# Optimization experiments

Hardware: AMD Instinct MI355X
Metric: run time of the kernel (lower is better)

## Reference

```python
import jax, jax.numpy as jnp
import numpy as np

B, P, C, H, W = 256, 512, 512, 7, 8
T = H * W  # 56
EPS = 1e-8


def setup_inputs() -> dict:
    key = jax.random.key(0)
    k1, k2, k3 = jax.random.split(key, 3)
    inp = jax.random.normal(k1, (B, C, H, W), dtype=jnp.float32)
    # xavier-uniform-like init for prototype (fan over last two dims as torch does)
    bound_p = float(np.sqrt(6.0 / (P + C * T)))
    prototype = jax.random.uniform(k2, (P, C, T), dtype=jnp.float32, minval=-bound_p, maxval=bound_p)
    bound_w = float(np.sqrt(6.0 / (C + 1)))
    fc_w = jax.random.uniform(k3, (1, C), dtype=jnp.float32, minval=-bound_w, maxval=bound_w)
    fc_b = jnp.zeros((1,), dtype=jnp.float32)
    return {"input": inp, "prototype": prototype, "fc_w": fc_w, "fc_b": fc_b}


def reference(input, prototype, fc_w, fc_b):
    # flatten spatial dims: (B, C, T)
    x = input.reshape(input.shape[0], input.shape[1], -1)
    # per-position cosine similarity over channel dim
    dots = jnp.einsum('bct,pct->bpt', x, prototype)          # (B, P, T)
    xn = jnp.linalg.norm(x, axis=1)                           # (B, T)
    pn = jnp.linalg.norm(prototype, axis=1)                   # (P, T)
    sim = dots / jnp.maximum(xn[:, None, :] * pn[None, :, :], EPS)
    att = jax.nn.softmax(sim, axis=-1)                        # (B, P, T)
    # attention-pooled elementwise product: (B, P, C)
    feat = jnp.einsum('bpt,bct,pct->bpc', att, x, prototype)
    # fc: Linear(C, 1) then relu, view to (B, P)
    out = jax.nn.relu(jnp.einsum('bpc,oc->bpo', feat, fc_w) + fc_b)
    return out.reshape(out.shape[0], out.shape[1])
```

## Files before the change

kernel.cpp:

```cpp
#include <hip/hip_runtime.h>
#include <hip/hip_bf16.h>
#include <math.h>

constexpr int kB = 256, kC = 512, kT = 56, kP = 512;
constexpr int kCT = kC * kT;

typedef short v4s __attribute__((ext_vector_type(4)));
typedef short v8s __attribute__((ext_vector_type(8)));
typedef float v4f __attribute__((ext_vector_type(4)));
typedef float v16f __attribute__((ext_vector_type(16)));

__device__ __forceinline__ unsigned pack_bf16(float a, float b) {
  __hip_bfloat16 ha = __float2bfloat16(a);
  __hip_bfloat16 hb = __float2bfloat16(b);
  unsigned short ua, ub;
  __builtin_memcpy(&ua, &ha, 2);
  __builtin_memcpy(&ub, &hb, 2);
  return (unsigned)ua | ((unsigned)ub << 16);
}

__device__ __forceinline__ v4s frag2(unsigned w0, unsigned w1) {
  unsigned u[2] = {w0, w1};
  v4s s;
  __builtin_memcpy(&s, u, 8);
  return s;
}

__device__ __forceinline__ v8s frag8(uint4 u) {
  v8s s;
  __builtin_memcpy(&s, &u, 16);
  return s;
}

#define GLOAD(gp, lp)                                                        \
  __builtin_amdgcn_global_load_lds(                                          \
      (const __attribute__((address_space(1))) unsigned*)(const unsigned*)(gp), \
      (__attribute__((address_space(3))) unsigned*)(unsigned*)(lp), 16, 0, 0)

__global__ __launch_bounds__(512) void prep_kernel(
    const float* __restrict__ x, const float* __restrict__ proto,
    const float* __restrict__ fcw,
    unsigned* __restrict__ xt, unsigned* __restrict__ xwt,
    unsigned* __restrict__ pt,
    float* __restrict__ xn, float* __restrict__ pn) {
  __shared__ float tile[128 * 57];
  __shared__ float fws[512];
  __shared__ float part[8][64];

  const int tid = threadIdx.x;
  const int n = blockIdx.x;
  const bool isx = (n < kB);
  const int row = isx ? n : (n - kB);
  const float* src = (isx ? x : proto) + (size_t)row * kCT;

  fws[tid] = fcw[tid & 511];

  const int g = tid >> 6, tt = tid & 63;
  float nacc = 0.f;

#pragma unroll 1
  for (int ch = 0; ch < 4; ++ch) {
    const float* csrc = src + ch * (128 * 56);
#pragma unroll
    for (int it = 0; it < 4; ++it) {
      const int idx = it * 512 + tid;
      if (idx < 1792) {
        const int f0 = idx * 4;
        float4 v = *(const float4*)(csrc + f0);
        int c = (int)(((unsigned)f0 * 74899u) >> 22);
        int t = f0 - c * 56;
        tile[c * 57 + t] = v.x;
        tile[c * 57 + t + 1] = v.y;
        tile[c * 57 + t + 2] = v.z;
        tile[c * 57 + t + 3] = v.w;
      }
    }
    __syncthreads();
    if (tt < 56) {
#pragma unroll
      for (int cc2 = 0; cc2 < 16; ++cc2) {
        float u = tile[(g * 16 + cc2) * 57 + tt];
        nacc = fmaf(u, u, nacc);
      }
    }
#pragma unroll
    for (int it = 0; it < 7; ++it) {
      const int id = it * 512 + tid;
      const int t = id >> 6;
      const int cw = id & 63;
      float g0 = tile[(2 * cw) * 57 + t];
      float g1 = tile[(2 * cw + 1) * 57 + t];
      unsigned wd = pack_bf16(g0, g1);
      if (isx) {
        const size_t o = ((size_t)(t * kB + row)) * 256 + ch * 64 + cw;
        const int c = ch * 128 + 2 * cw;
        xt[o] = wd;
        xwt[o] = pack_bf16(g0 * fws[c], g1 * fws[c + 1]);
      } else {
        pt[((size_t)(t * kP + row)) * 256 + ch * 64 + cw] = wd;
      }
    }
    __syncthreads();
  }

  part[g][tt] = nacc;
  __syncthreads();
  if (tid < 56) {
    float s = 0.f;
#pragma unroll
    for (int gg = 0; gg < 8; ++gg) s += part[gg][tid];
    float r = sqrtf(s);
    if (isx) xn[row * 56 + tid] = r; else pn[row * 56 + tid] = r;
  }
}

constexpr int TILE = 64 * 64;
constexpr int BUFW = 3 * TILE;

__global__ __launch_bounds__(256) void proto_gemm_kernel(
    const unsigned* __restrict__ xt, const unsigned* __restrict__ xwt,
    const unsigned* __restrict__ pt,
    const float* __restrict__ xn, const float* __restrict__ pn,
    float* __restrict__ part) {
  __shared__ __align__(16) unsigned lds[2 * BUFW];
  __shared__ float xnL[7 * 64], pnL[7 * 64];

  const int tid = threadIdx.x;
  const int l = tid & 63;
  const int w4 = tid >> 6;
  const int wm = w4 >> 1;
  const int wn = w4 & 1;

  int bid = (int)blockIdx.x;
  bid = (bid & 7) * 32 + (bid >> 3);
  const int b0 = (bid & 3) * 64;
  const int p0 = ((bid >> 2) & 7) * 64;
  const int tg = bid >> 5;

  for (int i = tid; i < 7 * 64; i += 256) {
    const int tl = i >> 6, r = i & 63;
    xnL[i] = xn[(b0 + r) * 56 + tg * 7 + tl];
    pnL[i] = pn[(p0 + r) * 56 + tg * 7 + tl];
  }

  const int l16 = l >> 4, s16 = l & 15;
  size_t xro[4], pro[4];
  int lo[4];
#pragma unroll
  for (int jj = 0; jj < 4; ++jj) {
    const int row = w4 * 16 + jj * 4 + l16;
    const int ch4 = (s16 ^ (row & 7)) * 4;
    xro[jj] = (size_t)(b0 + row) * 256 + ch4;
    pro[jj] = (size_t)(p0 + row) * 256 + ch4;
    lo[jj] = (w4 * 16 + jj * 4) * 64;
  }

  const int fr = l & 31;
  const int hi = l >> 5;
  const int sw4 = (l & 7) * 4;
  const int axb = (wm * 32 + fr) * 64;
  const int pxb = (wn * 32 + fr) * 64;

  v16f aD, aW, sac, nac;
#pragma unroll
  for (int i = 0; i < 16; ++i) { aD[i] = 0.f; aW[i] = 0.f; sac[i] = 0.f; nac[i] = 0.f; }

  auto STAGE = [&](int s, int buf) {
    const int t = tg * 7 + (s >> 2);
    const size_t xoff = (size_t)t * (kB * 256) + (size_t)((s & 3) * 64);
    const size_t poff = (size_t)t * (kP * 256) + (size_t)((s & 3) * 64);
    unsigned* lb = lds + buf * BUFW;
#pragma unroll
    for (int jj = 0; jj < 4; ++jj) {
      GLOAD(xt + xro[jj] + xoff, lb + lo[jj]);
      GLOAD(xwt + xro[jj] + xoff, lb + TILE + lo[jj]);
      GLOAD(pt + pro[jj] + poff, lb + 2 * TILE + lo[jj]);
    }
  };

  auto COMPUTE = [&](int s) {
    const unsigned* bx = lds + (s & 1) * BUFW;
#pragma unroll
    for (int ks = 0; ks < 8; ++ks) {
      const int col = (ks * 8 + hi * 4) ^ sw4;
      v8s xf = frag8(*(const uint4*)(bx + axb + col));
      v8s wf = frag8(*(const uint4*)(bx + TILE + axb + col));
      v8s pf = frag8(*(const uint4*)(bx + 2 * TILE + pxb + col));
      aD = __builtin_amdgcn_mfma_f32_32x32x16_bf16(xf, pf, aD, 0, 0, 0);
      aW = __builtin_amdgcn_mfma_f32_32x32x16_bf16(wf, pf, aW, 0, 0, 0);
    }
    if ((s & 3) == 3) {
      const int tl = s >> 2;
      const float pnv = pnL[tl * 64 + wn * 32 + fr];
#pragma unroll
      for (int i = 0; i < 16; ++i) {
        const int drow = (i & 3) + 8 * (i >> 2) + 4 * hi;
        float xnv = xnL[tl * 64 + wm * 32 + drow];
        float den = fmaxf(xnv * pnv, 1e-8f);
        float sim = aD[i] * __builtin_amdgcn_rcpf(den);
        float e = __expf(sim);
        sac[i] += e;
        nac[i] = fmaf(e, aW[i], nac[i]);
        aD[i] = 0.f;
        aW[i] = 0.f;
      }
    }
  };

  STAGE(0, 0);
  __syncthreads();

#pragma unroll 1
  for (int s = 0; s < 28; ++s) {
    if (s < 27) STAGE(s + 1, (s + 1) & 1);
    COMPUTE(s);
    __syncthreads();
  }

  float* psb = part + ((size_t)tg * 2 + 0) * 131072;
  float* pnb = part + ((size_t)tg * 2 + 1) * 131072;
#pragma unroll
  for (int i = 0; i < 16; ++i) {
    const int drow = (i & 3) + 8 * (i >> 2) + 4 * hi;
    const size_t o = (size_t)(b0 + wm * 32 + drow) * 512 + p0 + wn * 32 + fr;
    psb[o] = sac[i];
    pnb[o] = nac[i];
  }
}

__global__ __launch_bounds__(256) void merge_kernel(
    const float* __restrict__ part, const float* __restrict__ fcb,
    float* __restrict__ out) {
  const int pair = blockIdx.x * 256 + threadIdx.x;
  float S = 0.f, N = 0.f;
#pragma unroll
  for (int k = 0; k < 8; ++k) {
    S += part[((size_t)k * 2 + 0) * 131072 + pair];
    N += part[((size_t)k * 2 + 1) * 131072 + pair];
  }
  float o = N * __builtin_amdgcn_rcpf(S) + fcb[0];
  out[pair] = fmaxf(o, 0.f);
}

__global__ __launch_bounds__(1024) void proto_mfma_kernel(
    const float* __restrict__ x, const float* __restrict__ proto,
    const float* __restrict__ fcw, const float* __restrict__ fcb,
    float* __restrict__ out) {
  __shared__ unsigned xs[56 * 289];
  __shared__ unsigned ps[56 * 145];
  __shared__ unsigned pws[56 * 145];

  const int tid = threadIdx.x;
  const int l = tid & 63;
  const int w = tid >> 6;
  const int bq = w & 1;
  const int tq = w >> 1;
  const int t0 = tq * 7;

  const int n = blockIdx.y * 32 + blockIdx.x;
  const int p0 = (n >> 3) * 16;
  const int b0 = (n & 7) * 32;

  const bool act = (l < 56);
  const int lt = l;

  const int xbase0 = ((b0 + 2 * w + 0) * kC) * kT + lt;
  const int xbase1 = ((b0 + 2 * w + 1) * kC) * kT + lt;
  const int pbase = ((p0 + w) * kC) * kT + lt;

  const int arow = l & 15;
  const int q2 = (l >> 4) << 1;
  const int xoff = (bq * 16 + arow) * 9 + q2;
  const int poff = arow * 9 + q2;

  v4f acc[7][2];
#pragma unroll
  for (int ti = 0; ti < 7; ++ti) {
    acc[ti][0] = v4f{0.f, 0.f, 0.f, 0.f};
    acc[ti][1] = v4f{0.f, 0.f, 0.f, 0.f};
  }
  float xn2a = 0.f, xn2b = 0.f, pn2 = 0.f;

#pragma unroll 1
  for (int st = 0; st < 32; ++st) {
    const int k0 = st * 16;
    if (act) {
#pragma unroll
      for (int r = 0; r < 16; ++r) {
        const int cw = r & 7;
        const int c = k0 + 2 * cw;
        const int ga = ((r >> 3) ? xbase1 : xbase0) + c * kT;
        float g0 = x[ga], g1 = x[ga + kT];
        if (r >> 3) xn2b = fmaf(g0, g0, fmaf(g1, g1, xn2b));
        else xn2a = fmaf(g0, g0, fmaf(g1, g1, xn2a));
        xs[lt * 289 + (2 * w + (r >> 3)) * 9 + cw] = pack_bf16(g0, g1);
      }
#pragma unroll
      for (int cw = 0; cw < 8; ++cw) {
        const int c = k0 + 2 * cw;
        const int ga = pbase + c * kT;
        float g0 = proto[ga], g1 = proto[ga + kT];
        pn2 = fmaf(g0, g0, fmaf(g1, g1, pn2));
        ps[lt * 145 + w * 9 + cw] = pack_bf16(g0, g1);
        float f0 = fcw[c], f1 = fcw[c + 1];
        pws[lt * 145 + w * 9 + cw] = pack_bf16(g0 * f0, g1 * f1);
      }
    }
    __syncthreads();
#pragma unroll
    for (int ti = 0; ti < 7; ++ti) {
      const int t = t0 + ti;
      unsigned xw0 = xs[t * 289 + xoff];
      unsigned xw1 = xs[t * 289 + xoff + 1];
      unsigned pw0 = ps[t * 145 + poff];
      unsigned pw1 = ps[t * 145 + poff + 1];
      unsigned ww0 = pws[t * 145 + poff];
      unsigned ww1 = pws[t * 145 + poff + 1];
      v4s af = frag2(xw0, xw1);
      v4s bf = frag2(pw0, pw1);
      v4s wf = frag2(ww0, ww1);
      acc[ti][0] = __builtin_amdgcn_mfma_f32_16x16x16bf16_1k(af, bf, acc[ti][0], 0, 0, 0);
      acc[ti][1] = __builtin_amdgcn_mfma_f32_16x16x16bf16_1k(af, wf, acc[ti][1], 0, 0, 0);
    }
    __syncthreads();
  }

  float* xnorm = (float*)ps;
  float* pnorm = xnorm + 32 * 56;
  if (act) {
    xnorm[(2 * w + 0) * 56 + lt] = xn2a;
    xnorm[(2 * w + 1) * 56 + lt] = xn2b;
    pnorm[w * 56 + lt] = pn2;
  }
  __syncthreads();

  float* fm = (float*)xs;
  float* fsum = fm + 4096;
  float* fnum = fsum + 4096;
  const int pc = arow;
  const int qq = l >> 4;
#pragma unroll
  for (int i = 0; i < 4; ++i) {
    const int bl = bq * 16 + 4 * qq + i;
    float m = -3.0e38f;
    float sims[7];
#pragma unroll
    for (int ti = 0; ti < 7; ++ti) {
      const int t = t0 + ti;
      float den = fmaxf(sqrtf(xnorm[bl * 56 + t]) * sqrtf(pnorm[pc * 56 + t]), 1e-8f);
      float s = acc[ti][0][i] / den;
      sims[ti] = s;
      m = fmaxf(m, s);
    }
    float se = 0.f, nu = 0.f;
#pragma unroll
    for (int ti = 0; ti < 7; ++ti) {
      float e = __expf(sims[ti] - m);
      se += e;
      nu = fmaf(e, acc[ti][1][i], nu);
    }
    const int pair = bl * 16 + pc;
    fm[tq * 512 + pair] = m;
    fsum[tq * 512 + pair] = se;
    fnum[tq * 512 + pair] = nu;
  }
  __syncthreads();

  if (tid < 512) {
    float M = -3.0e38f;
#pragma unroll
    for (int k = 0; k < 8; ++k) M = fmaxf(M, fm[k * 512 + tid]);
    float S = 0.f, N = 0.f;
#pragma unroll
    for (int k = 0; k < 8; ++k) {
      float sc = __expf(fm[k * 512 + tid] - M);
      S = fmaf(fsum[k * 512 + tid], sc, S);
      N = fmaf(fnum[k * 512 + tid], sc, N);
    }
    float o = N / S + fcb[0];
    out[(b0 + (tid >> 4)) * kP + p0 + (tid & 15)] = fmaxf(o, 0.f);
  }
}

extern "C" void kernel_launch(void* const* d_in, const int* in_sizes, int n_in,
                              void* d_out, int out_size, void* d_ws, size_t ws_size,
                              hipStream_t stream) {
  const float* x = (const float*)d_in[0];
  const float* proto = (const float*)d_in[1];
  const float* fcw = (const float*)d_in[2];
  const float* fcb = (const float*)d_in[3];
  float* out = (float*)d_out;

  const size_t need = 67280896;
  if (ws_size >= need) {
    unsigned* xt = (unsigned*)d_ws;
    unsigned* xwt = xt + 3670016;
    unsigned* ptb = xt + 7340032;
    float* partb = (float*)(xt + 14680064);
    float* xnb = (float*)(xt + 16777216);
    float* pnb = xnb + 14336;

    hipLaunchKernelGGL(prep_kernel, dim3(kB + kP), dim3(512), 0, stream,
                       x, proto, fcw, xt, xwt, ptb, xnb, pnb);
    hipLaunchKernelGGL(proto_gemm_kernel, dim3(256), dim3(256), 0, stream,
                       xt, xwt, ptb, xnb, pnb, partb);
    hipLaunchKernelGGL(merge_kernel, dim3(512), dim3(256), 0, stream,
                       partb, fcb, out);
  } else {
    hipLaunchKernelGGL(proto_mfma_kernel, dim3(32, 8), dim3(1024), 0, stream,
                       x, proto, fcw, fcb, out);
  }
}
```

Before: 76.03 us.

## Split time groups finer, shrink K-tile, add triple-buffered async pipeline in gemm

```diff
diff --git a/kernel.cpp b/kernel.cpp
--- a/kernel.cpp
+++ b/kernel.cpp
@@ -114,16 +114,16 @@
   }
 }
 
-constexpr int TILE = 64 * 64;
-constexpr int BUFW = 3 * TILE;
-
-__global__ __launch_bounds__(256) void proto_gemm_kernel(
+constexpr int TILE = 64 * 32;
+constexpr int BUF = 3 * TILE;
+
+__global__ __launch_bounds__(256, 2) void proto_gemm_kernel(
     const unsigned* __restrict__ xt, const unsigned* __restrict__ xwt,
     const unsigned* __restrict__ pt,
     const float* __restrict__ xn, const float* __restrict__ pn,
     float* __restrict__ part) {
-  __shared__ __align__(16) unsigned lds[2 * BUFW];
-  __shared__ float xnL[7 * 64], pnL[7 * 64];
+  __shared__ __align__(16) unsigned lds[3 * BUF];
+  __shared__ float xnL[4 * 64], pnL[4 * 64];
 
   const int tid = threadIdx.x;
   const int l = tid & 63;
@@ -132,65 +132,66 @@
   const int wn = w4 & 1;
 
   int bid = (int)blockIdx.x;
-  bid = (bid & 7) * 32 + (bid >> 3);
+  bid = (bid & 7) * 56 + (bid >> 3);
   const int b0 = (bid & 3) * 64;
   const int p0 = ((bid >> 2) & 7) * 64;
   const int tg = bid >> 5;
 
-  for (int i = tid; i < 7 * 64; i += 256) {
-    const int tl = i >> 6, r = i & 63;
-    xnL[i] = xn[(b0 + r) * 56 + tg * 7 + tl];
-    pnL[i] = pn[(p0 + r) * 56 + tg * 7 + tl];
-  }
-
-  const int l16 = l >> 4, s16 = l & 15;
-  size_t xro[4], pro[4];
-  int lo[4];
-#pragma unroll
-  for (int jj = 0; jj < 4; ++jj) {
-    const int row = w4 * 16 + jj * 4 + l16;
-    const int ch4 = (s16 ^ (row & 7)) * 4;
-    xro[jj] = (size_t)(b0 + row) * 256 + ch4;
-    pro[jj] = (size_t)(p0 + row) * 256 + ch4;
-    lo[jj] = (w4 * 16 + jj * 4) * 64;
+  {
+    const int tl = tid >> 6, r = tid & 63;
+    xnL[tid] = xn[(b0 + r) * 56 + tg * 4 + tl];
+    pnL[tid] = pn[(p0 + r) * 56 + tg * 4 + tl];
+  }
+  __syncthreads();
+
+  const int lrow = l >> 3, lch = l & 7;
+  size_t xsrc[2], psrc[2];
+  int ldst[2];
+#pragma unroll
+  for (int j = 0; j < 2; ++j) {
+    const int row = w4 * 16 + j * 8 + lrow;
+    const int ch4 = ((lch ^ (row & 7))) * 4;
+    xsrc[j] = (size_t)(b0 + row) * 256 + ch4;
+    psrc[j] = (size_t)(p0 + row) * 256 + ch4;
+    ldst[j] = (w4 * 16 + j * 8) * 32;
   }
 
   const int fr = l & 31;
   const int hi = l >> 5;
-  const int sw4 = (l & 7) * 4;
-  const int axb = (wm * 32 + fr) * 64;
-  const int pxb = (wn * 32 + fr) * 64;
+  const int axb = (wm * 32 + fr) * 32;
+  const int pxb = (wn * 32 + fr) * 32;
+  const int frs = fr & 7;
 
   v16f aD, aW, sac, nac;
 #pragma unroll
   for (int i = 0; i < 16; ++i) { aD[i] = 0.f; aW[i] = 0.f; sac[i] = 0.f; nac[i] = 0.f; }
 
   auto STAGE = [&](int s, int buf) {
-    const int t = tg * 7 + (s >> 2);
-    const size_t xoff = (size_t)t * (kB * 256) + (size_t)((s & 3) * 64);
-    const size_t poff = (size_t)t * (kP * 256) + (size_t)((s & 3) * 64);
-    unsigned* lb = lds + buf * BUFW;
-#pragma unroll
-    for (int jj = 0; jj < 4; ++jj) {
-      GLOAD(xt + xro[jj] + xoff, lb + lo[jj]);
-      GLOAD(xwt + xro[jj] + xoff, lb + TILE + lo[jj]);
-      GLOAD(pt + pro[jj] + poff, lb + 2 * TILE + lo[jj]);
+    const int t = tg * 4 + (s >> 3);
+    const size_t xo = (size_t)t * (kB * 256) + (size_t)((s & 7) * 32);
+    const size_t po = (size_t)t * (kP * 256) + (size_t)((s & 7) * 32);
+    unsigned* lb = lds + buf * BUF;
+#pragma unroll
+    for (int j = 0; j < 2; ++j) {
+      GLOAD(xt + xsrc[j] + xo, lb + ldst[j]);
+      GLOAD(xwt + xsrc[j] + xo, lb + TILE + ldst[j]);
+      GLOAD(pt + psrc[j] + po, lb + 2 * TILE + ldst[j]);
     }
   };
 
-  auto COMPUTE = [&](int s) {
-    const unsigned* bx = lds + (s & 1) * BUFW;
-#pragma unroll
-    for (int ks = 0; ks < 8; ++ks) {
-      const int col = (ks * 8 + hi * 4) ^ sw4;
+  auto COMPUTE = [&](int s, int buf) {
+    const unsigned* bx = lds + buf * BUF;
+#pragma unroll
+    for (int ks = 0; ks < 4; ++ks) {
+      const int col = (((ks << 1) | hi) ^ frs) << 2;
       v8s xf = frag8(*(const uint4*)(bx + axb + col));
       v8s wf = frag8(*(const uint4*)(bx + TILE + axb + col));
       v8s pf = frag8(*(const uint4*)(bx + 2 * TILE + pxb + col));
       aD = __builtin_amdgcn_mfma_f32_32x32x16_bf16(xf, pf, aD, 0, 0, 0);
       aW = __builtin_amdgcn_mfma_f32_32x32x16_bf16(wf, pf, aW, 0, 0, 0);
     }
-    if ((s & 3) == 3) {
-      const int tl = s >> 2;
+    if ((s & 7) == 7) {
+      const int tl = s >> 3;
       const float pnv = pnL[tl * 64 + wn * 32 + fr];
 #pragma unroll
       for (int i = 0; i < 16; ++i) {
@@ -208,13 +209,20 @@
   };
 
   STAGE(0, 0);
-  __syncthreads();
-
+  STAGE(1, 1);
+
+  int c0 = 0, c1 = 1, c2 = 2;
 #pragma unroll 1
-  for (int s = 0; s < 28; ++s) {
-    if (s < 27) STAGE(s + 1, (s + 1) & 1);
-    COMPUTE(s);
-    __syncthreads();
+  for (int s = 0; s < 32; ++s) {
+    if (s < 30) STAGE(s + 2, c2);
+    if (s < 30)      asm volatile("s_waitcnt vmcnt(12)" ::: "memory");
+    else if (s == 30) asm volatile("s_waitcnt vmcnt(6)" ::: "memory");
+    else              asm volatile("s_waitcnt vmcnt(0)" ::: "memory");
+    __builtin_amdgcn_s_barrier();
+    __builtin_amdgcn_sched_barrier(0);
+    COMPUTE(s, c0);
+    __builtin_amdgcn_s_barrier();
+    const int tmp = c0; c0 = c1; c1 = c2; c2 = tmp;
   }
 
   float* psb = part + ((size_t)tg * 2 + 0) * 131072;
@@ -234,7 +242,7 @@
   const int pair = blockIdx.x * 256 + threadIdx.x;
   float S = 0.f, N = 0.f;
 #pragma unroll
-  for (int k = 0; k < 8; ++k) {
+  for (int k = 0; k < 14; ++k) {
     S += part[((size_t)k * 2 + 0) * 131072 + pair];
     N += part[((size_t)k * 2 + 1) * 131072 + pair];
   }
@@ -391,18 +399,18 @@
   const float* fcb = (const float*)d_in[3];
   float* out = (float*)d_out;
 
-  const size_t need = 67280896;
+  const size_t need = 73572352;
   if (ws_size >= need) {
     unsigned* xt = (unsigned*)d_ws;
     unsigned* xwt = xt + 3670016;
     unsigned* ptb = xt + 7340032;
     float* partb = (float*)(xt + 14680064);
-    float* xnb = (float*)(xt + 16777216);
+    float* xnb = (float*)(xt + 18350080);
     float* pnb = xnb + 14336;
 
     hipLaunchKernelGGL(prep_kernel, dim3(kB + kP), dim3(512), 0, stream,
                        x, proto, fcw, xt, xwt, ptb, xnb, pnb);
-    hipLaunchKernelGGL(proto_gemm_kernel, dim3(256), dim3(256), 0, stream,
+    hipLaunchKernelGGL(proto_gemm_kernel, dim3(448), dim3(256), 0, stream,
                        xt, xwt, ptb, xnb, pnb, partb);
     hipLaunchKernelGGL(merge_kernel, dim3(512), dim3(256), 0, stream,
                        partb, fcb, out);
```

Result: faster. 65.62 us (-13.7%).
